# Performance work log

Hardware: AMD Instinct MI355X
Metric: run time of the kernel (lower is better)

## Reference

```python
import jax, jax.numpy as jnp
import numpy as np

N_NODES = 50000
N_EDGES = 800000
IN_CH = 256
HID_CH = 128


def setup_inputs() -> dict:
    key = jax.random.key(0)
    k1, k2, k3, k4, k5 = jax.random.split(key, 5)
    x = jax.random.normal(k1, (N_NODES, IN_CH), dtype=jnp.float32)
    edge_index = jax.random.randint(k2, (2, N_EDGES), 0, N_NODES, dtype=jnp.int64)
    edge_weight = jax.random.uniform(k3, (N_EDGES,), dtype=jnp.float32)
    W = jax.random.normal(k4, (IN_CH, HID_CH), dtype=jnp.float32) * (1.0 / np.sqrt(IN_CH))
    b = jnp.zeros((HID_CH,), dtype=jnp.float32)
    alpha = jnp.full((HID_CH,), 0.25, dtype=jnp.float32)  # PReLU default init
    return {"x": x, "edge_index": edge_index, "edge_weight": edge_weight,
            "W": W, "b": b, "alpha": alpha}


def reference(x, edge_index, edge_weight, W, b, alpha):
    """GCNConv (with self-loops + symmetric normalization) followed by PReLU."""
    N = x.shape[0]
    row, col = edge_index[0], edge_index[1]
    # add self-loops with weight 1 (PyG gcn_norm default, add_self_loops=True)
    loop = jnp.arange(N, dtype=row.dtype)
    row = jnp.concatenate([row, loop])
    col = jnp.concatenate([col, loop])
    ew = jnp.concatenate([edge_weight, jnp.ones((N,), dtype=edge_weight.dtype)])
    # degree from edge weights, scattered at destination (col)
    deg = jax.ops.segment_sum(ew, col, num_segments=N)
    deg_inv_sqrt = jnp.where(deg > 0, jax.lax.rsqrt(deg), 0.0)
    norm = deg_inv_sqrt[row] * ew * deg_inv_sqrt[col]  # [E+N]
    # linear transform then gather-scale-scatter aggregation
    h = x @ W                               # [N, HID]
    msg = h[row] * norm[:, None]            # [E+N, HID]
    out = jax.ops.segment_sum(msg, col, num_segments=N) + b
    # PReLU with per-channel slope
    return jnp.where(out >= 0, out, alpha * out)
```

## Files before the change

kernel.cpp:

```cpp
#include <hip/hip_runtime.h>

#define NN 50000
#define NE 800000
#define KD 256
#define CD 128
#define NB 196
#define GEMM_BLOCKS 782
#define HIST4_BLOCKS 782
#define META_BLOCKS 782

typedef __attribute__((ext_vector_type(8))) short short8;
typedef __attribute__((ext_vector_type(4))) float floatx4;
typedef __attribute__((ext_vector_type(2))) float floatx2;

__device__ inline unsigned short f2bf(float f) {
    unsigned u = __float_as_uint(f);
    unsigned r = (u + 0x7FFFu + ((u >> 16) & 1u)) >> 16;
    return (unsigned short)r;
}
__device__ inline float bf2f_lo(unsigned u) { return __uint_as_float(u << 16); }
__device__ inline float bf2f_hi(unsigned u) { return __uint_as_float(u & 0xFFFF0000u); }

__global__ __launch_bounds__(256) void prep(const float* __restrict__ W,
                                            unsigned short* __restrict__ Wt,
                                            unsigned* __restrict__ packedAll,
                                            unsigned long long* __restrict__ state) {
    __shared__ unsigned short t[32][33];
    if (blockIdx.x < NB) {
        const int g = blockIdx.x * 256 + threadIdx.x;
        if (g < NN) {
#pragma unroll
            for (int c = 0; c < 4; c++) packedAll[(size_t)c * NN + g] = 0u;
        }
        if (blockIdx.x == 0) {
            for (int i = threadIdx.x; i < NB * 8; i += 256) state[i] = 0ull;
        }
        return;
    }
    const int b2 = blockIdx.x - NB;
    const int bk = (b2 & 7) * 32;
    const int bn = (b2 >> 3) * 32;
    const int tx = threadIdx.x & 31;
    const int ty = threadIdx.x >> 5;
#pragma unroll
    for (int i = 0; i < 32; i += 8)
        t[ty + i][tx] = f2bf(W[(size_t)(bk + ty + i) * CD + bn + tx]);
    __syncthreads();
#pragma unroll
    for (int i = 0; i < 32; i += 8)
        Wt[(size_t)(bn + ty + i) * KD + bk + tx] = t[tx][ty + i];
}

__global__ __launch_bounds__(256) void fused_gemm_hist(
        const float* __restrict__ x, const unsigned short* __restrict__ Wt,
        unsigned short* __restrict__ hb,
        const int* __restrict__ col, const float* __restrict__ ew,
        unsigned* __restrict__ packedAll, unsigned short* __restrict__ rank) {
    if (blockIdx.x >= GEMM_BLOCKS) {
        const int e0 = ((blockIdx.x - GEMM_BLOCKS) * 256 + threadIdx.x) * 4;
        if (e0 < NE) {
            const int4 c4 = *(const int4*)(col + e0);
            const float4 w4 = *(const float4*)(ew + e0);
            unsigned* packed = packedAll + (size_t)((threadIdx.x >> 6) & 3) * NN;
            const unsigned o0 = atomicAdd(&packed[c4.x], (1u << 24) + (unsigned)(w4.x * 262144.0f));
            const unsigned o1 = atomicAdd(&packed[c4.y], (1u << 24) + (unsigned)(w4.y * 262144.0f));
            const unsigned o2 = atomicAdd(&packed[c4.z], (1u << 24) + (unsigned)(w4.z * 262144.0f));
            const unsigned o3 = atomicAdd(&packed[c4.w], (1u << 24) + (unsigned)(w4.w * 262144.0f));
            ushort4 r;
            r.x = (unsigned short)(o0 >> 24);
            r.y = (unsigned short)(o1 >> 24);
            r.z = (unsigned short)(o2 >> 24);
            r.w = (unsigned short)(o3 >> 24);
            *(ushort4*)(rank + e0) = r;
        }
        return;
    }

    const int tid  = threadIdx.x;
    const int wave = tid >> 6;
    const int lane = tid & 63;
    const int row0 = blockIdx.x * 64;
    const int m0   = wave * 16;
    const int lr   = lane & 15;
    const int quad = lane >> 4;

    const int grow_a = row0 + m0 + lr;
    const bool ok = grow_a < NN;
    const float* xp = x + (size_t)grow_a * KD + quad * 8;
    const unsigned short* wp = Wt + (size_t)lr * KD + quad * 8;

    floatx4 acc[8];
#pragma unroll
    for (int nt = 0; nt < 8; nt++) acc[nt] = (floatx4){0.f, 0.f, 0.f, 0.f};

#pragma unroll 2
    for (int kt = 0; kt < 8; kt++) {
        union { short8 v; unsigned short us[8]; } av;
        if (ok) {
            const float4 f0 = *(const float4*)(xp + kt * 32);
            const float4 f1 = *(const float4*)(xp + kt * 32 + 4);
            av.us[0] = f2bf(f0.x); av.us[1] = f2bf(f0.y);
            av.us[2] = f2bf(f0.z); av.us[3] = f2bf(f0.w);
            av.us[4] = f2bf(f1.x); av.us[5] = f2bf(f1.y);
            av.us[6] = f2bf(f1.z); av.us[7] = f2bf(f1.w);
        } else {
            av.v = (short8){0,0,0,0,0,0,0,0};
        }
        short8 b[8];
#pragma unroll
        for (int nt = 0; nt < 8; nt++)
            b[nt] = *(const short8*)(wp + (size_t)nt * 16 * KD + kt * 32);
#pragma unroll
        for (int nt = 0; nt < 8; nt++)
            acc[nt] = __builtin_amdgcn_mfma_f32_16x16x32_bf16(av.v, b[nt], acc[nt], 0, 0, 0);
    }

#pragma unroll
    for (int i = 0; i < 4; i++) {
        const int grow = row0 + m0 + quad * 4 + i;
        if (grow < NN) {
            unsigned short* hp = hb + (size_t)grow * CD + lr;
#pragma unroll
            for (int nt = 0; nt < 8; nt++)
                hp[nt * 16] = f2bf(acc[nt][i]);
        }
    }
}

__global__ __launch_bounds__(256) void scan_lookback(
        const unsigned* __restrict__ packedAll,
        unsigned long long* __restrict__ state,
        int* __restrict__ start, int4* __restrict__ base4,
        float* __restrict__ dinv) {
    __shared__ int sm[256];
    __shared__ int sbase;
    const int t = threadIdx.x;
    const int b = blockIdx.x;
    const int g = b * 256 + t;

    int cc[4] = {0, 0, 0, 0};
    unsigned lowsum = 0;
    int v = 0;
    if (g < NN) {
#pragma unroll
        for (int c = 0; c < 4; c++) {
            unsigned p = packedAll[(size_t)c * NN + g];
            cc[c] = (int)(p >> 24);
            lowsum += p & 0xFFFFFFu;
            v += cc[c];
        }
    }
    sm[t] = v;
    __syncthreads();
#pragma unroll
    for (int off = 1; off < 256; off <<= 1) {
        int u = (t >= off) ? sm[t - off] : 0;
        __syncthreads();
        sm[t] += u;
        __syncthreads();
    }
    const int incl = sm[t];
    const int total = sm[255];

    if (t == 0) {
        unsigned long long post =
            ((b == 0 ? 2ull : 1ull) << 32) | (unsigned)total;
        __hip_atomic_store(&state[(size_t)b * 8], post,
                           __ATOMIC_RELAXED, __HIP_MEMORY_SCOPE_AGENT);
        if (b == 0) sbase = 0;
    }
    if (b > 0 && t < 64) {
        long long run = 0;
        int i = b - 1;
        while (true) {
            const int idx = i - t;
            unsigned long long s = (idx >= 0)
                ? __hip_atomic_load(&state[(size_t)idx * 8],
                                    __ATOMIC_RELAXED, __HIP_MEMORY_SCOPE_AGENT)
                : (2ull << 32);
            const unsigned st = (unsigned)(s >> 32);
            const unsigned long long b0m = __ballot(st == 0u);
            const unsigned long long b2m = __ballot(st == 2u);
            if (b2m) {
                const int L = __ffsll((long long)b2m) - 1;
                const unsigned long long below =
                    (L == 63) ? ~0ull : ((1ull << (L + 1)) - 1ull);
                if (b0m & below) { __builtin_amdgcn_s_sleep(1); continue; }
                unsigned val = (t <= L) ? (unsigned)s : 0u;
#pragma unroll
                for (int o = 32; o; o >>= 1) val += __shfl_xor(val, o);
                run += val;
                break;
            } else if (b0m) {
                const int L0 = __ffsll((long long)b0m) - 1;
                unsigned val = (t < L0) ? (unsigned)s : 0u;
#pragma unroll
                for (int o = 32; o; o >>= 1) val += __shfl_xor(val, o);
                run += val;
                i -= L0;
                if (L0 == 0) __builtin_amdgcn_s_sleep(1);
            } else {
                unsigned val = (unsigned)s;
#pragma unroll
                for (int o = 32; o; o >>= 1) val += __shfl_xor(val, o);
                run += val;
                i -= 64;
            }
        }
        if (t == 0) {
            __hip_atomic_store(&state[(size_t)b * 8],
                               (2ull << 32) | (unsigned)(run + total),
                               __ATOMIC_RELAXED, __HIP_MEMORY_SCOPE_AGENT);
            sbase = (int)run;
        }
    }
    __syncthreads();
    const int base = sbase;

    if (g < NN) {
        const int s = base + (incl - v);
        start[g] = s;
        base4[g] = make_int4(s, s + cc[0], s + cc[0] + cc[1], s + cc[0] + cc[1] + cc[2]);
        float degs = (float)lowsum * (1.0f / 262144.0f);
        dinv[g] = rsqrtf(1.0f + degs);
    }
    if (g == 0) start[NN] = NE;
}

__global__ __launch_bounds__(256) void meta_write(const int* __restrict__ row,
                                                  const int* __restrict__ col,
                                                  const float* __restrict__ ew,
                                                  const unsigned short* __restrict__ rank,
                                                  const int4* __restrict__ base4,
                                                  const float* __restrict__ dinv,
                                                  unsigned* __restrict__ meta) {
    const int e0 = (blockIdx.x * 256 + threadIdx.x) * 4;
    if (e0 >= NE) return;
    const int4 c4 = *(const int4*)(col + e0);
    const int4 r4 = *(const int4*)(row + e0);
    const float4 w4 = *(const float4*)(ew + e0);
    const ushort4 k4 = *(const ushort4*)(rank + e0);
    const int cs[4] = {c4.x, c4.y, c4.z, c4.w};
    const int rs[4] = {r4.x, r4.y, r4.z, r4.w};
    const float wsv[4] = {w4.x, w4.y, w4.z, w4.w};
    const unsigned short ks[4] = {k4.x, k4.y, k4.z, k4.w};
#pragma unroll
    for (int j = 0; j < 4; j++) {
        const int e = e0 + j;
        const int copy = (e >> 8) & 3;
        const int4 b4 = base4[cs[j]];
        const int base = (copy == 0) ? b4.x : (copy == 1) ? b4.y
                       : (copy == 2) ? b4.z : b4.w;
        const unsigned short wbf = f2bf(dinv[rs[j]] * wsv[j]);
        meta[base + ks[j]] = ((unsigned)wbf << 16) | (unsigned)rs[j];
    }
}

__global__ __launch_bounds__(256) void aggregate(const int* __restrict__ start,
                                                 const unsigned* __restrict__ meta,
                                                 const unsigned short* __restrict__ hb,
                                                 const float* __restrict__ dinv,
                                                 const float* __restrict__ bias,
                                                 const float* __restrict__ alpha,
                                                 float* __restrict__ out) {
    int n = blockIdx.x * 4 + (threadIdx.x >> 6);
    if (n >= NN) return;
    n = __builtin_amdgcn_readfirstlane(n);
    const int lane = threadIdx.x & 63;
    const int s = __builtin_amdgcn_readfirstlane(start[n]);
    const int e = __builtin_amdgcn_readfirstlane(start[n + 1]);

    float A0[8], A1[8];
#pragma unroll
    for (int j = 0; j < 8; j++) { A0[j] = 0.f; A1[j] = 0.f; }

    int i = s;
    for (; i + 8 <= e; i += 8) {
        unsigned m[8], u[8];
#pragma unroll
        for (int j = 0; j < 8; j++) m[j] = __builtin_nontemporal_load(meta + i + j);
#pragma unroll
        for (int j = 0; j < 8; j++)
            u[j] = *(const unsigned*)(hb + (size_t)(m[j] & 0xFFFFu) * CD + lane * 2);
#pragma unroll
        for (int j = 0; j < 8; j++) {
            float w = __uint_as_float(m[j] & 0xFFFF0000u);
            A0[j] = fmaf(w, bf2f_lo(u[j]), A0[j]);
            A1[j] = fmaf(w, bf2f_hi(u[j]), A1[j]);
        }
    }
    for (; i < e; i++) {
        unsigned m = __builtin_nontemporal_load(meta + i);
        unsigned u = *(const unsigned*)(hb + (size_t)(m & 0xFFFFu) * CD + lane * 2);
        float w = __uint_as_float(m & 0xFFFF0000u);
        A0[0] = fmaf(w, bf2f_lo(u), A0[0]);
        A1[0] = fmaf(w, bf2f_hi(u), A1[0]);
    }
#pragma unroll
    for (int j = 1; j < 8; j++) { A0[0] += A0[j]; A1[0] += A1[j]; }

    const float dc = dinv[n];
    unsigned us = *(const unsigned*)(hb + (size_t)n * CD + lane * 2);
    const int ch = lane * 2;
    float o0 = dc * A0[0] + dc * dc * bf2f_lo(us) + bias[ch];
    float o1 = dc * A1[0] + dc * dc * bf2f_hi(us) + bias[ch + 1];
    o0 = o0 >= 0.f ? o0 : alpha[ch] * o0;
    o1 = o1 >= 0.f ? o1 : alpha[ch + 1] * o1;
    floatx2 o; o.x = o0; o.y = o1;
    __builtin_nontemporal_store(o, (floatx2*)(out + (size_t)n * CD + ch));
}

extern "C" void kernel_launch(void* const* d_in, const int* in_sizes, int n_in,
                              void* d_out, int out_size, void* d_ws, size_t ws_size,
                              hipStream_t stream) {
    const float* x     = (const float*)d_in[0];
    const int*   eidx  = (const int*)d_in[1];
    const float* ew    = (const float*)d_in[2];
    const float* Wm    = (const float*)d_in[3];
    const float* bias  = (const float*)d_in[4];
    const float* alpha = (const float*)d_in[5];
    const int* row = eidx;
    const int* col = eidx + NE;

    float* out = (float*)d_out;

    char* ws = (char*)d_ws;
    unsigned* packedAll = (unsigned*)(ws);
    int*   start    = (int*)(ws + 800000);
    float* dinv     = (float*)(ws + 1000064);
    unsigned short* rank = (unsigned short*)(ws + 1200064);
    int4*  base4    = (int4*)(ws + 2800064);
    unsigned* meta  = (unsigned*)(ws + 3600064);
    unsigned short* Wt = (unsigned short*)(ws + 6800064);
    unsigned long long* state = (unsigned long long*)(ws + 6865600);
    unsigned short* hb = (unsigned short*)(ws + 6878208);

    prep          <<<NB + 32, 256, 0, stream>>>(Wm, Wt, packedAll, state);
    fused_gemm_hist<<<GEMM_BLOCKS + HIST4_BLOCKS, 256, 0, stream>>>(
                        x, Wt, hb, col, ew, packedAll, rank);
    scan_lookback <<<NB, 256, 0, stream>>>(packedAll, state, start, base4, dinv);
    meta_write    <<<META_BLOCKS, 256, 0, stream>>>(row, col, ew, rank, base4, dinv, meta);
    aggregate     <<<(NN + 3) / 4, 256, 0, stream>>>(start, meta, hb, dinv, bias, alpha, out);
}
```

Baseline: 209.9 us.

## Stage W tiles in LDS, preload x rows, and use one-edge-per-thread histogram

The GEMM part now loads all eight bf16-converted x fragments up front and stages W in shared memory in 64-wide K chunks. The MFMA B operands are then read from LDS instead of being re-fetched from global memory by every wave. The histogram blocks change from four edges per thread to one edge per thread, using 3125 blocks, with the packed-copy selection keyed by block rather than wave. This trades more LDS traffic, block barriers and register pressure for less redundant global loads and more latency hiding in the atomic phase.

```diff
diff --git a/kernel.cpp b/kernel.cpp
--- a/kernel.cpp
+++ b/kernel.cpp
@@ -6,7 +6,7 @@
 #define CD 128
 #define NB 196
 #define GEMM_BLOCKS 782
-#define HIST4_BLOCKS 782
+#define HIST_BLOCKS 3125
 #define META_BLOCKS 782
 
 typedef __attribute__((ext_vector_type(8))) short short8;
@@ -56,22 +56,16 @@
         unsigned short* __restrict__ hb,
         const int* __restrict__ col, const float* __restrict__ ew,
         unsigned* __restrict__ packedAll, unsigned short* __restrict__ rank) {
+    __shared__ unsigned short Bs[128][68];
+
     if (blockIdx.x >= GEMM_BLOCKS) {
-        const int e0 = ((blockIdx.x - GEMM_BLOCKS) * 256 + threadIdx.x) * 4;
-        if (e0 < NE) {
-            const int4 c4 = *(const int4*)(col + e0);
-            const float4 w4 = *(const float4*)(ew + e0);
-            unsigned* packed = packedAll + (size_t)((threadIdx.x >> 6) & 3) * NN;
-            const unsigned o0 = atomicAdd(&packed[c4.x], (1u << 24) + (unsigned)(w4.x * 262144.0f));
-            const unsigned o1 = atomicAdd(&packed[c4.y], (1u << 24) + (unsigned)(w4.y * 262144.0f));
-            const unsigned o2 = atomicAdd(&packed[c4.z], (1u << 24) + (unsigned)(w4.z * 262144.0f));
-            const unsigned o3 = atomicAdd(&packed[c4.w], (1u << 24) + (unsigned)(w4.w * 262144.0f));
-            ushort4 r;
-            r.x = (unsigned short)(o0 >> 24);
-            r.y = (unsigned short)(o1 >> 24);
-            r.z = (unsigned short)(o2 >> 24);
-            r.w = (unsigned short)(o3 >> 24);
-            *(ushort4*)(rank + e0) = r;
+        const int hblk = blockIdx.x - GEMM_BLOCKS;
+        const int e = hblk * 256 + threadIdx.x;
+        if (e < NE) {
+            unsigned* packed = packedAll + (size_t)(hblk & 3) * NN;
+            unsigned p = (1u << 24) + (unsigned)(ew[e] * 262144.0f);
+            unsigned old = atomicAdd(&packed[col[e]], p);
+            rank[e] = (unsigned short)(old >> 24);
         }
         return;
     }
@@ -87,32 +81,50 @@
     const int grow_a = row0 + m0 + lr;
     const bool ok = grow_a < NN;
     const float* xp = x + (size_t)grow_a * KD + quad * 8;
-    const unsigned short* wp = Wt + (size_t)lr * KD + quad * 8;
-
-    floatx4 acc[8];
-#pragma unroll
-    for (int nt = 0; nt < 8; nt++) acc[nt] = (floatx4){0.f, 0.f, 0.f, 0.f};
-
-#pragma unroll 2
+
+    union { short8 v; unsigned short us[8]; } avs[8];
+#pragma unroll
     for (int kt = 0; kt < 8; kt++) {
-        union { short8 v; unsigned short us[8]; } av;
         if (ok) {
             const float4 f0 = *(const float4*)(xp + kt * 32);
             const float4 f1 = *(const float4*)(xp + kt * 32 + 4);
-            av.us[0] = f2bf(f0.x); av.us[1] = f2bf(f0.y);
-            av.us[2] = f2bf(f0.z); av.us[3] = f2bf(f0.w);
-            av.us[4] = f2bf(f1.x); av.us[5] = f2bf(f1.y);
-            av.us[6] = f2bf(f1.z); av.us[7] = f2bf(f1.w);
+            avs[kt].us[0] = f2bf(f0.x); avs[kt].us[1] = f2bf(f0.y);
+            avs[kt].us[2] = f2bf(f0.z); avs[kt].us[3] = f2bf(f0.w);
+            avs[kt].us[4] = f2bf(f1.x); avs[kt].us[5] = f2bf(f1.y);
+            avs[kt].us[6] = f2bf(f1.z); avs[kt].us[7] = f2bf(f1.w);
         } else {
-            av.v = (short8){0,0,0,0,0,0,0,0};
-        }
-        short8 b[8];
-#pragma unroll
-        for (int nt = 0; nt < 8; nt++)
-            b[nt] = *(const short8*)(wp + (size_t)nt * 16 * KD + kt * 32);
-#pragma unroll
-        for (int nt = 0; nt < 8; nt++)
-            acc[nt] = __builtin_amdgcn_mfma_f32_16x16x32_bf16(av.v, b[nt], acc[nt], 0, 0, 0);
+            avs[kt].v = (short8){0,0,0,0,0,0,0,0};
+        }
+    }
+
+    floatx4 acc[8];
+#pragma unroll
+    for (int nt = 0; nt < 8; nt++) acc[nt] = (floatx4){0.f, 0.f, 0.f, 0.f};
+
+#pragma unroll
+    for (int kq = 0; kq < 4; kq++) {
+        if (kq) __syncthreads();
+#pragma unroll
+        for (int r8 = 0; r8 < 4; r8++) {
+            const int idx  = r8 * 256 + tid;
+            const int rown = idx >> 3;
+            const int koff = (idx & 7) * 8;
+            *(short8*)&Bs[rown][koff] =
+                *(const short8*)(Wt + (size_t)rown * KD + kq * 64 + koff);
+        }
+        __syncthreads();
+#pragma unroll
+        for (int kt2 = 0; kt2 < 2; kt2++) {
+            const int kt = kq * 2 + kt2;
+            short8 b[8];
+#pragma unroll
+            for (int nt = 0; nt < 8; nt++)
+                b[nt] = *(const short8*)&Bs[nt * 16 + lr][kt2 * 32 + quad * 8];
+#pragma unroll
+            for (int nt = 0; nt < 8; nt++)
+                acc[nt] = __builtin_amdgcn_mfma_f32_16x16x32_bf16(
+                              avs[kt].v, b[nt], acc[nt], 0, 0, 0);
+        }
     }
 
 #pragma unroll
@@ -336,7 +348,7 @@
     unsigned short* hb = (unsigned short*)(ws + 6878208);
 
     prep          <<<NB + 32, 256, 0, stream>>>(Wm, Wt, packedAll, state);
-    fused_gemm_hist<<<GEMM_BLOCKS + HIST4_BLOCKS, 256, 0, stream>>>(
+    fused_gemm_hist<<<GEMM_BLOCKS + HIST_BLOCKS, 256, 0, stream>>>(
                         x, Wt, hb, col, ew, packedAll, rank);
     scan_lookback <<<NB, 256, 0, stream>>>(packedAll, state, start, base4, dinv);
     meta_write    <<<META_BLOCKS, 256, 0, stream>>>(row, col, ew, rank, base4, dinv, meta);
```

New measurement: 188.3 us. 10.3% less time.
